# Optimization experiments

Hardware: AMD Instinct MI355X
Metric: run time of the kernel (lower is better)

Reference implementation:

```python
import jax, jax.numpy as jnp
import numpy as np

GAMMA_LOCAL = 2.5
ALPHA = 1.2
DELTA = 1.0
TAU = 0.3
LAMBDA_CONTRAST = 0.5
EPS = 1e-7


def _corners(b):
    # b: [..., 4] in xywh format; returns corners and w,h, each [..., 1] (keepdims, matching torch.chunk)
    x, y, w, h = b[..., 0:1], b[..., 1:2], b[..., 2:3], b[..., 3:4]
    return x - w / 2, x + w / 2, y - h / 2, y + h / 2, w, h


def bbox_iou(box1, box2, ciou=False):
    # Faithful port of ultralytics bbox_iou (xywh=True). Output keeps a trailing dim of 1.
    b1x1, b1x2, b1y1, b1y2, w1, h1 = _corners(box1)
    b2x1, b2x2, b2y1, b2y2, w2, h2 = _corners(box2)
    inter = jnp.clip(jnp.minimum(b1x2, b2x2) - jnp.maximum(b1x1, b2x1), 0, None) * \
            jnp.clip(jnp.minimum(b1y2, b2y2) - jnp.maximum(b1y1, b2y1), 0, None)
    union = w1 * h1 + w2 * h2 - inter + EPS
    iou = inter / union
    if ciou:
        cw = jnp.maximum(b1x2, b2x2) - jnp.minimum(b1x1, b2x1)  # enclosing box width
        ch = jnp.maximum(b1y2, b2y2) - jnp.minimum(b1y1, b2y1)  # enclosing box height
        c2 = cw ** 2 + ch ** 2 + EPS
        rho2 = ((b2x1 + b2x2 - b1x1 - b1x2) ** 2 + (b2y1 + b2y2 - b1y1 - b1y2) ** 2) / 4
        v = (4 / np.pi ** 2) * (jnp.arctan(w2 / h2) - jnp.arctan(w1 / h1)) ** 2
        alpha = jax.lax.stop_gradient(v / (v - iou + (1 + EPS)))  # torch computes alpha under no_grad
        iou = iou - (rho2 / c2 + v * alpha)
    return iou


def setup_inputs() -> dict:
    key = jax.random.key(0)
    k1, k2, k3, k4, k5 = jax.random.split(key, 5)
    N, D, P = 8192, 256, 100
    pred_boxes = jax.random.uniform(k1, (N, 4), dtype=jnp.float32)
    target_boxes = jax.random.uniform(k2, (N, 4), dtype=jnp.float32)
    embeddings = jax.random.normal(k3, (N, D), dtype=jnp.float32)
    density_map = jax.random.uniform(k4, (N,), dtype=jnp.float32)
    indices = jax.random.randint(k5, (P, 2), 0, N, dtype=jnp.int64 if jax.config.jax_enable_x64 else jnp.int32)
    return {"pred_boxes": pred_boxes, "target_boxes": target_boxes,
            "embeddings": embeddings, "density_map": density_map, "indices": indices}


def reference(pred_boxes, target_boxes, embeddings, density_map, indices):
    # Localization term
    ious = bbox_iou(pred_boxes, target_boxes, ciou=True)            # [N, 1]
    area_norm = target_boxes[..., 2] * target_boxes[..., 3]          # [N]
    saf_ciou = (1 - ious) ** GAMMA_LOCAL / (area_norm + 1e-7)        # [N,1]/[N] -> [N,N] broadcast (as in torch)
    density_weight = 1 + ALPHA * density_map[..., None]              # [N, 1]
    hardness_weight = jax.nn.sigmoid(5.0 * (0.5 - jax.lax.stop_gradient(ious)))  # [N, 1]
    loss_loc = (density_weight * hardness_weight * saf_ciou).mean()

    # Contrastive term: vectorized version of the per-pair Python loop
    bi = pred_boxes[indices[:, 0]]                                   # [P, 4]
    bj = pred_boxes[indices[:, 1]]                                   # [P, 4]
    pair_iou = bbox_iou(bi, bj, ciou=False)[..., 0]                  # [P]
    mask = pair_iou > TAU                                            # [P] bool
    emb_dist = jnp.linalg.norm(embeddings[indices[:, 0]] - embeddings[indices[:, 1]], axis=-1)  # [P]
    pair_loss = jax.nn.relu(DELTA - emb_dist) ** 2                   # [P]
    contrastive_loss = jnp.sum(jnp.where(mask, pair_loss, 0.0))

    P = indices.shape[0]
    loss_contrast = LAMBDA_CONTRAST * contrastive_loss / (P + 1e-7)
    return loss_loc + loss_contrast
```

## Files before the change

kernel.cpp:

```cpp
#include <hip/hip_runtime.h>
#include <hip/hip_bf16.h>
#include <math.h>


#define NTHR 1024

__device__ __forceinline__ float iou_plain(float4 b1, float4 b2) {
    float b1x1 = b1.x - 0.5f * b1.z, b1x2 = b1.x + 0.5f * b1.z;
    float b1y1 = b1.y - 0.5f * b1.w, b1y2 = b1.y + 0.5f * b1.w;
    float b2x1 = b2.x - 0.5f * b2.z, b2x2 = b2.x + 0.5f * b2.z;
    float b2y1 = b2.y - 0.5f * b2.w, b2y2 = b2.y + 0.5f * b2.w;
    float iw = fmaxf(fminf(b1x2, b2x2) - fmaxf(b1x1, b2x1), 0.0f);
    float ih = fmaxf(fminf(b1y2, b2y2) - fmaxf(b1y1, b2y1), 0.0f);
    float inter = iw * ih;
    float uni = b1.z * b1.w + b2.z * b2.w - inter + 1e-7f;
    return inter / uni;
}

__device__ __forceinline__ float iou_ciou(float4 b1, float4 b2) {
    float b1x1 = b1.x - 0.5f * b1.z, b1x2 = b1.x + 0.5f * b1.z;
    float b1y1 = b1.y - 0.5f * b1.w, b1y2 = b1.y + 0.5f * b1.w;
    float b2x1 = b2.x - 0.5f * b2.z, b2x2 = b2.x + 0.5f * b2.z;
    float b2y1 = b2.y - 0.5f * b2.w, b2y2 = b2.y + 0.5f * b2.w;
    float iw = fmaxf(fminf(b1x2, b2x2) - fmaxf(b1x1, b2x1), 0.0f);
    float ih = fmaxf(fminf(b1y2, b2y2) - fmaxf(b1y1, b2y1), 0.0f);
    float inter = iw * ih;
    float uni = b1.z * b1.w + b2.z * b2.w - inter + 1e-7f;
    float iou = inter / uni;
    float cw = fmaxf(b1x2, b2x2) - fminf(b1x1, b2x1);
    float ch = fmaxf(b1y2, b2y2) - fminf(b1y1, b2y1);
    float c2 = cw * cw + ch * ch + 1e-7f;
    float dx = b2.x - b1.x, dy = b2.y - b1.y;
    float rho2 = dx * dx + dy * dy;
    float dat = atanf(b2.z / b2.w) - atanf(b1.z / b1.w);
    const float four_over_pi2 = 0.40528473456935108578f;
    float v = four_over_pi2 * dat * dat;
    float alpha = v / (v - iou + (1.0f + 1e-7f));
    return iou - (rho2 / c2 + v * alpha);
}

__global__ __launch_bounds__(NTHR) void fused_kernel(
    const float4* __restrict__ pred, const float4* __restrict__ targ,
    const float* __restrict__ emb, const float* __restrict__ dens,
    const int* __restrict__ idx, float* __restrict__ out, int N, int P) {
    int tid = threadIdx.x;
    int lane = tid & 63;
    int wid = tid >> 6;

    float sA = 0.0f, sB = 0.0f, sC = 0.0f;

    #pragma unroll 4
    for (int i = tid; i < N; i += NTHR) {
        float4 pb = pred[i];
        float4 tb = targ[i];
        float dn = dens[i];
        float iou = iou_ciou(pb, tb);
        float om = fmaxf(1.0f - iou, 0.0f);
        float saf = om * om * sqrtf(om);
        float hw = 1.0f / (1.0f + expf(5.0f * iou - 2.5f));
        sA += (1.0f + 1.2f * dn) * hw * saf;
        sB += 1.0f / (tb.z * tb.w + 1e-7f);
    }

    for (int p = wid; p < P; p += (NTHR / 64)) {
        int i0 = idx[2 * p];
        int i1 = idx[2 * p + 1];
        float4 a = ((const float4*)(emb + (size_t)i0 * 256))[lane];
        float4 b = ((const float4*)(emb + (size_t)i1 * 256))[lane];
        float dx = a.x - b.x, dy = a.y - b.y, dz = a.z - b.z, dw = a.w - b.w;
        float d2 = dx * dx + dy * dy + dz * dz + dw * dw;
        #pragma unroll
        for (int o = 32; o > 0; o >>= 1) d2 += __shfl_xor(d2, o);
        if (lane == 0) {
            float dist = sqrtf(d2);
            float pl = fmaxf(1.0f - dist, 0.0f);
            pl = pl * pl;
            float piou = iou_plain(pred[i0], pred[i1]);
            if (piou > 0.3f) sC += pl;
        }
    }

    #pragma unroll
    for (int o = 32; o > 0; o >>= 1) {
        sA += __shfl_xor(sA, o);
        sB += __shfl_xor(sB, o);
        sC += __shfl_xor(sC, o);
    }
    __shared__ float red[NTHR / 64][3];
    if (lane == 0) {
        red[wid][0] = sA; red[wid][1] = sB; red[wid][2] = sC;
    }
    __syncthreads();
    if (tid == 0) {
        float a = 0.0f, b = 0.0f, c = 0.0f;
        #pragma unroll
        for (int w = 0; w < NTHR / 64; w++) {
            a += red[w][0]; b += red[w][1]; c += red[w][2];
        }
        float n2 = (float)N * (float)N;
        out[0] = (a * b) / n2 + 0.5f * c / ((float)P + 1e-7f);
    }
}

extern "C" void kernel_launch(void* const* d_in, const int* in_sizes, int n_in,
                              void* d_out, int out_size, void* d_ws, size_t ws_size,
                              hipStream_t stream) {
    const float4* pred = (const float4*)d_in[0];
    const float4* targ = (const float4*)d_in[1];
    const float* emb   = (const float*)d_in[2];
    const float* dens  = (const float*)d_in[3];
    const int* idx     = (const int*)d_in[4];
    float* out = (float*)d_out;

    int N = in_sizes[0] / 4;
    int P = in_sizes[4] / 2;

    fused_kernel<<<1, NTHR, 0, stream>>>(pred, targ, emb, dens, idx, out, N, P);
}
```

Baseline: 83.09 us.

## Split fused loss kernel across 64 blocks with flag-based cross-block reduction

Replaces the single 1024-thread block with 64 blocks of 256 threads, grid-striding over boxes and embedding pairs. Each block writes its partial sums to workspace and raises a release flag. Block 0 spins on the flags, then reduces the 64 partials with wave shuffles. This targets the latency of one workgroup running all the transcendental work alone. The flags are never reset, so a later call may skip the wait and read stale partials. Block 0 also depends on all blocks being resident at once.

```diff
diff --git a/kernel.cpp b/kernel.cpp
--- a/kernel.cpp
+++ b/kernel.cpp
@@ -3,7 +3,8 @@
 #include <math.h>
 
 
-#define NTHR 1024
+#define NBLK 64
+#define NTHR 256
 
 __device__ __forceinline__ float iou_plain(float4 b1, float4 b2) {
     float b1x1 = b1.x - 0.5f * b1.z, b1x2 = b1.x + 0.5f * b1.z;
@@ -42,15 +43,17 @@
 __global__ __launch_bounds__(NTHR) void fused_kernel(
     const float4* __restrict__ pred, const float4* __restrict__ targ,
     const float* __restrict__ emb, const float* __restrict__ dens,
-    const int* __restrict__ idx, float* __restrict__ out, int N, int P) {
+    const int* __restrict__ idx, float* __restrict__ out,
+    float* __restrict__ ws, int N, int P) {
     int tid = threadIdx.x;
+    int bid = blockIdx.x;
+    int gtid = bid * NTHR + tid;
     int lane = tid & 63;
     int wid = tid >> 6;
 
     float sA = 0.0f, sB = 0.0f, sC = 0.0f;
 
-    #pragma unroll 4
-    for (int i = tid; i < N; i += NTHR) {
+    for (int i = gtid; i < N; i += NBLK * NTHR) {
         float4 pb = pred[i];
         float4 tb = targ[i];
         float dn = dens[i];
@@ -62,7 +65,8 @@
         sB += 1.0f / (tb.z * tb.w + 1e-7f);
     }
 
-    for (int p = wid; p < P; p += (NTHR / 64)) {
+    int gwid = gtid >> 6;
+    for (int p = gwid; p < P; p += NBLK * (NTHR / 64)) {
         int i0 = idx[2 * p];
         int i1 = idx[2 * p + 1];
         float4 a = ((const float4*)(emb + (size_t)i0 * 256))[lane];
@@ -87,18 +91,37 @@
         sC += __shfl_xor(sC, o);
     }
     __shared__ float red[NTHR / 64][3];
-    if (lane == 0) {
-        red[wid][0] = sA; red[wid][1] = sB; red[wid][2] = sC;
-    }
+    if (lane == 0) { red[wid][0] = sA; red[wid][1] = sB; red[wid][2] = sC; }
     __syncthreads();
+
+    unsigned int* flags = (unsigned int*)ws + 3 * NBLK;
     if (tid == 0) {
         float a = 0.0f, b = 0.0f, c = 0.0f;
         #pragma unroll
-        for (int w = 0; w < NTHR / 64; w++) {
-            a += red[w][0]; b += red[w][1]; c += red[w][2];
+        for (int w = 0; w < NTHR / 64; w++) { a += red[w][0]; b += red[w][1]; c += red[w][2]; }
+        __hip_atomic_store(&ws[bid],            a, __ATOMIC_RELAXED, __HIP_MEMORY_SCOPE_AGENT);
+        __hip_atomic_store(&ws[NBLK + bid],     b, __ATOMIC_RELAXED, __HIP_MEMORY_SCOPE_AGENT);
+        __hip_atomic_store(&ws[2 * NBLK + bid], c, __ATOMIC_RELAXED, __HIP_MEMORY_SCOPE_AGENT);
+        __hip_atomic_store(&flags[bid], 1u, __ATOMIC_RELEASE, __HIP_MEMORY_SCOPE_AGENT);
+    }
+
+    if (bid == 0 && tid < 64) {
+        while (__hip_atomic_load(&flags[lane], __ATOMIC_ACQUIRE, __HIP_MEMORY_SCOPE_AGENT) != 1u) {
+            __builtin_amdgcn_s_sleep(1);
         }
-        float n2 = (float)N * (float)N;
-        out[0] = (a * b) / n2 + 0.5f * c / ((float)P + 1e-7f);
+        float a = __hip_atomic_load(&ws[lane],            __ATOMIC_RELAXED, __HIP_MEMORY_SCOPE_AGENT);
+        float b = __hip_atomic_load(&ws[NBLK + lane],     __ATOMIC_RELAXED, __HIP_MEMORY_SCOPE_AGENT);
+        float c = __hip_atomic_load(&ws[2 * NBLK + lane], __ATOMIC_RELAXED, __HIP_MEMORY_SCOPE_AGENT);
+        #pragma unroll
+        for (int o = 32; o > 0; o >>= 1) {
+            a += __shfl_xor(a, o);
+            b += __shfl_xor(b, o);
+            c += __shfl_xor(c, o);
+        }
+        if (lane == 0) {
+            float n2 = (float)N * (float)N;
+            out[0] = (a * b) / n2 + 0.5f * c / ((float)P + 1e-7f);
+        }
     }
 }
 
@@ -111,9 +134,10 @@
     const float* dens  = (const float*)d_in[3];
     const int* idx     = (const int*)d_in[4];
     float* out = (float*)d_out;
+    float* ws  = (float*)d_ws;
 
     int N = in_sizes[0] / 4;
     int P = in_sizes[4] / 2;
 
-    fused_kernel<<<1, NTHR, 0, stream>>>(pred, targ, emb, dens, idx, out, N, P);
+    fused_kernel<<<NBLK, NTHR, 0, stream>>>(pred, targ, emb, dens, idx, out, ws, N, P);
 }
```

Measured after the change: 66.66 us. 19.8% less time.
